# Optimization experiments

Measured on AMD Instinct MI355X. Metric: run time of the kernel, lower is better.

Reference implementation:

```python
import jax, jax.numpy as jnp
import numpy as np

NUM_HEADS = 8
WIN = 8

def setup_inputs() -> dict:
    key = jax.random.key(0)
    k1, k2, k3 = jax.random.split(key, 3)
    B, H, W, C = 4, 256, 256, 256
    x = jax.random.normal(k1, (B, H, W, C), dtype=jnp.float32)
    w_qkv = jax.random.normal(k2, (C, 3 * C), dtype=jnp.float32) * (1.0 / np.sqrt(C))
    b_qkv = jnp.zeros((3 * C,), dtype=jnp.float32)
    w_proj = jax.random.normal(k3, (C, C), dtype=jnp.float32) * (1.0 / np.sqrt(C))
    b_proj = jnp.zeros((C,), dtype=jnp.float32)
    return {"x": x, "w_qkv": w_qkv, "b_qkv": b_qkv, "w_proj": w_proj, "b_proj": b_proj}

def reference(x, w_qkv, b_qkv, w_proj, b_proj):
    B, H, W, C = x.shape
    ws = WIN
    pad_h = (ws - H % ws) % ws
    pad_w = (ws - W % ws) % ws
    if pad_h > 0 or pad_w > 0:
        x = jnp.pad(x, ((0, 0), (0, pad_h), (0, pad_w), (0, 0)), mode='reflect')
        H, W = H + pad_h, W + pad_w
    Ho, Wo = H - pad_h, W - pad_w
    # window partition: [B, H//ws, ws, W//ws, ws, C] -> [nW, ws*ws, C]
    xw = x.reshape(B, H // ws, ws, W // ws, ws, C)
    xw = xw.transpose(0, 1, 3, 2, 4, 5).reshape(-1, ws * ws, C)
    head_dim = C // NUM_HEADS
    scale = head_dim ** (-0.5)
    qkv = xw @ w_qkv + b_qkv  # [nW, T, 3C]
    qkv = qkv.reshape(-1, ws * ws, 3, NUM_HEADS, head_dim).transpose(2, 0, 3, 1, 4)
    q, k, v = qkv[0], qkv[1], qkv[2]  # each [nW, h, T, d]
    attn = jnp.einsum('whtd,whsd->whts', q, k) * scale
    attn = jax.nn.softmax(attn, axis=-1)
    o = jnp.einsum('whts,whsd->whtd', attn, v)
    o = o.transpose(0, 2, 1, 3).reshape(-1, ws * ws, C)
    o = o @ w_proj + b_proj
    # window merge
    o = o.reshape(B, H // ws, W // ws, ws, ws, C)
    o = o.transpose(0, 1, 3, 2, 4, 5).reshape(B, H, W, C)
    return o[:, :Ho, :Wo, :]
```

## Files before the change

### kernel.cpp

```cpp
#include <hip/hip_runtime.h>
#include <hip/hip_bf16.h>

typedef __attribute__((ext_vector_type(8))) short short8;
typedef __attribute__((ext_vector_type(4))) short short4v;
typedef __attribute__((ext_vector_type(4))) float f32x4;

#define MFMA(a, b, c) __builtin_amdgcn_mfma_f32_16x16x32_bf16(a, b, c, 0, 0, 0)
#define XS(t, c) (((t) << 8) + ((c) ^ (((t) & 7) << 3)))

extern "C" __device__ float __ocml_native_exp2_f32(float);
#define EXP2(x) __ocml_native_exp2_f32(x)

__device__ __forceinline__ unsigned int pk2(float lo, float hi) {
    union { __hip_bfloat162 h2; unsigned int u; } cv;
    cv.h2 = __float22bfloat162_rn(make_float2(lo, hi));
    return cv.u;
}

__device__ __forceinline__ unsigned short f2bf1(float f) {
    unsigned int u = __float_as_uint(f);
    u += 0x7FFFu + ((u >> 16) & 1u);
    return (unsigned short)(u >> 16);
}

__device__ __forceinline__ short4v u2s4(uint2 p) {
    union { uint2 u; short4v s; } t; t.u = p; return t.s;
}

#if __has_builtin(__builtin_amdgcn_mfma_f32_16x16x16bf16_1k)
__device__ __forceinline__ f32x4 mfma16(uint2 a, uint2 b, f32x4 c) {
    return __builtin_amdgcn_mfma_f32_16x16x16bf16_1k(u2s4(a), u2s4(b), c, 0, 0, 0);
}
#else
__device__ __forceinline__ short8 zfrag(uint2 p) {
    union { unsigned int u[4]; short8 s; } t;
    t.u[0] = p.x; t.u[1] = p.y; t.u[2] = 0u; t.u[3] = 0u;
    return t.s;
}
__device__ __forceinline__ f32x4 mfma16(uint2 a, uint2 b, f32x4 c) {
    return MFMA(zfrag(a), zfrag(b), c);
}
#endif

#define SCLF 0.25500566631879443f

__global__ void prep_w(const float* __restrict__ wqkv, const float* __restrict__ wproj,
                       unsigned short* __restrict__ wT) {
    int idx = blockIdx.x * 256 + threadIdx.x;
    if (idx < 196608) {
        const int frag   = idx >> 9;
        const int within = idx & 511;
        const int lane = within >> 3, j = within & 7;
        const int ks = frag & 7;
        const int dt = (frag >> 3) & 1;
        const int hh = (frag >> 4) & 7;
        const int m  = frag >> 7;
        const int n = m * 256 + hh * 32 + dt * 16 + (lane & 15);
        const int k = ks * 32 + ((lane >> 4) << 3) + j;
        float v = wqkv[k * 768 + n];
        if (m == 0) v *= SCLF;
        wT[idx] = f2bf1(v);
    } else {
        const int r = idx - 196608;
        const int frag = r >> 9;
        const int within = r & 511;
        const int lane = within >> 3, j = within & 7;
        const int ks = frag & 7;
        const int nt = (frag >> 3) & 1;
        const int hh = frag >> 4;
        const int n = hh * 32 + nt * 16 + (lane & 15);
        const int k = ks * 32 + ((lane >> 4) << 3) + j;
        wT[idx] = f2bf1(wproj[k * 256 + n]);
    }
}

__global__ __launch_bounds__(512, 2)
void winattn(const float* __restrict__ x,
             const float* __restrict__ bqkv,
             const float* __restrict__ bproj,
             const unsigned short* __restrict__ wpk,
             const unsigned short* __restrict__ wpj,
             float* __restrict__ out)
{
    __shared__ unsigned short smem[64 * 256];

    const int tid  = threadIdx.x;
    const int h    = tid >> 6;
    const int lane = tid & 63;
    const int g    = lane >> 4;
    const int q16  = lane & 15;

    const int bid  = blockIdx.x;
    const int widx = (bid & 7) * 512 + (bid >> 3);
    const int b  = widx >> 10;
    const int wh = (widx >> 5) & 31;
    const int ww = widx & 31;

    {
        const int t  = tid >> 3;
        const int c0 = (tid & 7) << 3;
        const int hr = (wh << 3) + (t >> 3);
        const int wc = (ww << 3) + (t & 7);
        const float* rowp = x + (((size_t)b * 256 + hr) * 256 + wc) * 256;
        #pragma unroll
        for (int u = 0; u < 4; ++u) {
            const int c = c0 + (u << 6);
            const float4 f0 = *reinterpret_cast<const float4*>(rowp + c);
            const float4 f1 = *reinterpret_cast<const float4*>(rowp + c + 4);
            union { unsigned int u4[4]; short8 s; } pv;
            pv.u4[0] = pk2(f0.x, f0.y); pv.u4[1] = pk2(f0.z, f0.w);
            pv.u4[2] = pk2(f1.x, f1.y); pv.u4[3] = pk2(f1.z, f1.w);
            *reinterpret_cast<short8*>(&smem[XS(t, c)]) = pv.s;
        }
    }
    __syncthreads();

    const unsigned short* wh0 = wpk + ((size_t)h << 13);
    const int loff = lane << 3;

    uint2 pq[2][4], pkk[2][4], pv2[2][4];
    #pragma unroll
    for (int half = 0; half < 2; ++half) {
        f32x4 acc[3][2][2];
        #pragma unroll
        for (int dt = 0; dt < 2; ++dt) {
            const float4 bbq = *reinterpret_cast<const float4*>(bqkv + h * 32 + dt * 16 + (g << 2));
            const float4 bbk = *reinterpret_cast<const float4*>(bqkv + 256 + h * 32 + dt * 16 + (g << 2));
            const float bv = bqkv[512 + h * 32 + dt * 16 + q16];
            const f32x4 iq = {bbq.x * SCLF, bbq.y * SCLF, bbq.z * SCLF, bbq.w * SCLF};
            const f32x4 ik = {bbk.x, bbk.y, bbk.z, bbk.w};
            const f32x4 ivv = {bv, bv, bv, bv};
            #pragma unroll
            for (int t2 = 0; t2 < 2; ++t2) {
                acc[0][dt][t2] = iq; acc[1][dt][t2] = ik; acc[2][dt][t2] = ivv;
            }
        }
        #pragma unroll
        for (int ks = 0; ks < 8; ++ks) {
            const int kc = ks << 5;
            short8 xf[2];
            #pragma unroll
            for (int t2 = 0; t2 < 2; ++t2)
                xf[t2] = *reinterpret_cast<const short8*>(
                    &smem[XS(((half << 1) + t2) * 16 + q16, kc + (g << 3))]);
            #pragma unroll
            for (int m = 0; m < 3; ++m) {
                #pragma unroll
                for (int dt = 0; dt < 2; ++dt) {
                    const short8 wf = *reinterpret_cast<const short8*>(
                        wh0 + (((size_t)m << 16) | (((dt << 3) + ks) << 9)) + loff);
                    #pragma unroll
                    for (int t2 = 0; t2 < 2; ++t2)
                        acc[m][dt][t2] = (m < 2) ? MFMA(wf, xf[t2], acc[m][dt][t2])
                                                 : MFMA(xf[t2], wf, acc[m][dt][t2]);
                }
            }
        }
        #pragma unroll
        for (int dt = 0; dt < 2; ++dt) {
            #pragma unroll
            for (int t2 = 0; t2 < 2; ++t2) {
                const int tt = (half << 1) + t2;
                const f32x4 aq = acc[0][dt][t2];
                pq[dt][tt]  = make_uint2(pk2(aq[0], aq[1]), pk2(aq[2], aq[3]));
                const f32x4 ak = acc[1][dt][t2];
                pkk[dt][tt] = make_uint2(pk2(ak[0], ak[1]), pk2(ak[2], ak[3]));
                const f32x4 av = acc[2][dt][t2];
                pv2[dt][tt] = make_uint2(pk2(av[0], av[1]), pk2(av[2], av[3]));
            }
        }
    }

    const f32x4 fz = {0.f, 0.f, 0.f, 0.f};
    uint2 ppk[4][4];
    float inv4[4];
    #pragma unroll
    for (int qt = 0; qt < 4; ++qt) {
        f32x4 st[4];
        #pragma unroll
        for (int kt = 0; kt < 4; ++kt) st[kt] = fz;
        #pragma unroll
        for (int dt = 0; dt < 2; ++dt)
            #pragma unroll
            for (int kt = 0; kt < 4; ++kt)
                st[kt] = mfma16(pkk[dt][kt], pq[dt][qt], st[kt]);
        float sum = 0.f;
        #pragma unroll
        for (int kt = 0; kt < 4; ++kt) {
            const float e0 = EXP2(st[kt][0]), e1 = EXP2(st[kt][1]);
            const float e2 = EXP2(st[kt][2]), e3 = EXP2(st[kt][3]);
            sum += (e0 + e1) + (e2 + e3);
            ppk[kt][qt] = make_uint2(pk2(e0, e1), pk2(e2, e3));
        }
        sum += __shfl_xor(sum, 16);
        sum += __shfl_xor(sum, 32);
        inv4[qt] = 1.f / sum;
    }

    f32x4 ot[2][4];
    #pragma unroll
    for (int dt = 0; dt < 2; ++dt)
        #pragma unroll
        for (int tt = 0; tt < 4; ++tt) ot[dt][tt] = fz;
    #pragma unroll
    for (int kt = 0; kt < 4; ++kt)
        #pragma unroll
        for (int tt = 0; tt < 4; ++tt)
            #pragma unroll
            for (int dt = 0; dt < 2; ++dt)
                ot[dt][tt] = mfma16(pv2[dt][kt], ppk[kt][tt], ot[dt][tt]);

    __syncthreads();
    #pragma unroll
    for (int dt = 0; dt < 2; ++dt)
        #pragma unroll
        for (int tt = 0; tt < 4; ++tt) {
            const float iv = inv4[tt];
            const int tok = tt * 16 + q16;
            const int d   = h * 32 + dt * 16 + (g << 2);
            const uint2 pv = make_uint2(pk2(ot[dt][tt][0] * iv, ot[dt][tt][1] * iv),
                                        pk2(ot[dt][tt][2] * iv, ot[dt][tt][3] * iv));
            *reinterpret_cast<uint2*>(&smem[XS(tok, d)]) = pv;
        }
    __syncthreads();

    f32x4 pacc[4][2];
    {
        float bpv[2];
        #pragma unroll
        for (int nt = 0; nt < 2; ++nt) bpv[nt] = bproj[h * 32 + nt * 16 + q16];
        #pragma unroll
        for (int mt = 0; mt < 4; ++mt)
            #pragma unroll
            for (int nt = 0; nt < 2; ++nt) {
                const f32x4 ib = {bpv[nt], bpv[nt], bpv[nt], bpv[nt]};
                pacc[mt][nt] = ib;
            }
    }
    const unsigned short* wpjh = wpj + ((size_t)h << 13);
    #pragma unroll
    for (int ks = 0; ks < 8; ++ks) {
        const int kc = ks << 5;
        short8 of[4], wf[2];
        #pragma unroll
        for (int mt = 0; mt < 4; ++mt)
            of[mt] = *reinterpret_cast<const short8*>(&smem[XS(mt * 16 + q16, kc + (g << 3))]);
        #pragma unroll
        for (int nt = 0; nt < 2; ++nt)
            wf[nt] = *reinterpret_cast<const short8*>(wpjh + (((nt << 3) + ks) << 9) + loff);
        #pragma unroll
        for (int mt = 0; mt < 4; ++mt)
            #pragma unroll
            for (int nt = 0; nt < 2; ++nt)
                pacc[mt][nt] = MFMA(of[mt], wf[nt], pacc[mt][nt]);
    }
    {
        float* obase = out + (((size_t)b * 256 + (wh << 3) + (g >> 1)) * 256
                              + (ww << 3) + ((g & 1) << 2)) * 256 + h * 32 + q16;
        #pragma unroll
        for (int mt = 0; mt < 4; ++mt)
            #pragma unroll
            for (int r = 0; r < 4; ++r)
                #pragma unroll
                for (int nt = 0; nt < 2; ++nt)
                    obase[mt * 131072 + r * 256 + nt * 16] = pacc[mt][nt][r];
    }
}

extern "C" void kernel_launch(void* const* d_in, const int* in_sizes, int n_in,
                              void* d_out, int out_size, void* d_ws, size_t ws_size,
                              hipStream_t stream) {
    const float* x     = (const float*)d_in[0];
    const float* wqkv  = (const float*)d_in[1];
    const float* bqkv  = (const float*)d_in[2];
    const float* wproj = (const float*)d_in[3];
    const float* bproj = (const float*)d_in[4];
    float* out = (float*)d_out;
    unsigned short* wT = (unsigned short*)d_ws;

    prep_w<<<1024, 256, 0, stream>>>(wqkv, wproj, wT);
    winattn<<<4096, 512, 0, stream>>>(x, bqkv, bproj, wT, wT + 196608, out);
}
```

Measured before the change: 291.1 us.

## Use 4-wave blocks with each wave processing two heads sequentially

The block drops from 8 waves to 4. Each wave now loops over two heads for the QKV projection and attention, and writes its per-head outputs into a separate LDS region. That removes one barrier between attention and the projection stage. The output projection is re-partitioned so each wave computes 64 output columns, and the wproj prepack layout is changed to match. LDS per block doubles to 64KB and per-wave work doubles, which may cut occupancy and latency hiding in exchange for fewer waves and less sync.

```diff
diff --git a/kernel.cpp b/kernel.cpp
--- a/kernel.cpp
+++ b/kernel.cpp
@@ -66,15 +66,14 @@
         const int within = r & 511;
         const int lane = within >> 3, j = within & 7;
         const int ks = frag & 7;
-        const int nt = (frag >> 3) & 1;
-        const int hh = frag >> 4;
-        const int n = hh * 32 + nt * 16 + (lane & 15);
+        const int cb = frag >> 3;
+        const int n = cb * 16 + (lane & 15);
         const int k = ks * 32 + ((lane >> 4) << 3) + j;
         wT[idx] = f2bf1(wproj[k * 256 + n]);
     }
 }
 
-__global__ __launch_bounds__(512, 2)
+__global__ __launch_bounds__(256, 2)
 void winattn(const float* __restrict__ x,
              const float* __restrict__ bqkv,
              const float* __restrict__ bproj,
@@ -82,10 +81,10 @@
              const unsigned short* __restrict__ wpj,
              float* __restrict__ out)
 {
-    __shared__ unsigned short smem[64 * 256];
+    __shared__ unsigned short smem[32768];
 
     const int tid  = threadIdx.x;
-    const int h    = tid >> 6;
+    const int wid  = tid >> 6;
     const int lane = tid & 63;
     const int g    = lane >> 4;
     const int q16  = lane & 15;
@@ -97,14 +96,14 @@
     const int ww = widx & 31;
 
     {
-        const int t  = tid >> 3;
-        const int c0 = (tid & 7) << 3;
+        const int t  = tid >> 2;
+        const int c0 = (tid & 3) << 3;
         const int hr = (wh << 3) + (t >> 3);
         const int wc = (ww << 3) + (t & 7);
         const float* rowp = x + (((size_t)b * 256 + hr) * 256 + wc) * 256;
         #pragma unroll
-        for (int u = 0; u < 4; ++u) {
-            const int c = c0 + (u << 6);
+        for (int u = 0; u < 8; ++u) {
+            const int c = c0 + (u << 5);
             const float4 f0 = *reinterpret_cast<const float4*>(rowp + c);
             const float4 f1 = *reinterpret_cast<const float4*>(rowp + c + 4);
             union { unsigned int u4[4]; short8 s; } pv;
@@ -115,154 +114,158 @@
     }
     __syncthreads();
 
-    const unsigned short* wh0 = wpk + ((size_t)h << 13);
+    const f32x4 fz = {0.f, 0.f, 0.f, 0.f};
     const int loff = lane << 3;
 
-    uint2 pq[2][4], pkk[2][4], pv2[2][4];
-    #pragma unroll
-    for (int half = 0; half < 2; ++half) {
-        f32x4 acc[3][2][2];
-        #pragma unroll
-        for (int dt = 0; dt < 2; ++dt) {
-            const float4 bbq = *reinterpret_cast<const float4*>(bqkv + h * 32 + dt * 16 + (g << 2));
-            const float4 bbk = *reinterpret_cast<const float4*>(bqkv + 256 + h * 32 + dt * 16 + (g << 2));
-            const float bv = bqkv[512 + h * 32 + dt * 16 + q16];
-            const f32x4 iq = {bbq.x * SCLF, bbq.y * SCLF, bbq.z * SCLF, bbq.w * SCLF};
-            const f32x4 ik = {bbk.x, bbk.y, bbk.z, bbk.w};
-            const f32x4 ivv = {bv, bv, bv, bv};
-            #pragma unroll
-            for (int t2 = 0; t2 < 2; ++t2) {
-                acc[0][dt][t2] = iq; acc[1][dt][t2] = ik; acc[2][dt][t2] = ivv;
-            }
-        }
-        #pragma unroll
-        for (int ks = 0; ks < 8; ++ks) {
-            const int kc = ks << 5;
-            short8 xf[2];
-            #pragma unroll
-            for (int t2 = 0; t2 < 2; ++t2)
-                xf[t2] = *reinterpret_cast<const short8*>(
-                    &smem[XS(((half << 1) + t2) * 16 + q16, kc + (g << 3))]);
-            #pragma unroll
-            for (int m = 0; m < 3; ++m) {
-                #pragma unroll
-                for (int dt = 0; dt < 2; ++dt) {
-                    const short8 wf = *reinterpret_cast<const short8*>(
-                        wh0 + (((size_t)m << 16) | (((dt << 3) + ks) << 9)) + loff);
+    #pragma unroll 1
+    for (int p = 0; p < 2; ++p) {
+        const int h = (p << 2) + wid;
+        const unsigned short* wh0 = wpk + ((size_t)h << 13);
+
+        uint2 pq[2][4], pkk[2][4], pv2[2][4];
+        #pragma unroll
+        for (int half = 0; half < 2; ++half) {
+            f32x4 acc[3][2][2];
+            #pragma unroll
+            for (int dt = 0; dt < 2; ++dt) {
+                const float4 bbq = *reinterpret_cast<const float4*>(bqkv + h * 32 + dt * 16 + (g << 2));
+                const float4 bbk = *reinterpret_cast<const float4*>(bqkv + 256 + h * 32 + dt * 16 + (g << 2));
+                const float bv = bqkv[512 + h * 32 + dt * 16 + q16];
+                const f32x4 iq = {bbq.x * SCLF, bbq.y * SCLF, bbq.z * SCLF, bbq.w * SCLF};
+                const f32x4 ik = {bbk.x, bbk.y, bbk.z, bbk.w};
+                const f32x4 ivv = {bv, bv, bv, bv};
+                #pragma unroll
+                for (int t2 = 0; t2 < 2; ++t2) {
+                    acc[0][dt][t2] = iq; acc[1][dt][t2] = ik; acc[2][dt][t2] = ivv;
+                }
+            }
+            #pragma unroll
+            for (int ks = 0; ks < 8; ++ks) {
+                const int kc = ks << 5;
+                short8 xf[2];
+                #pragma unroll
+                for (int t2 = 0; t2 < 2; ++t2)
+                    xf[t2] = *reinterpret_cast<const short8*>(
+                        &smem[XS(((half << 1) + t2) * 16 + q16, kc + (g << 3))]);
+                #pragma unroll
+                for (int m = 0; m < 3; ++m) {
                     #pragma unroll
-                    for (int t2 = 0; t2 < 2; ++t2)
-                        acc[m][dt][t2] = (m < 2) ? MFMA(wf, xf[t2], acc[m][dt][t2])
-                                                 : MFMA(xf[t2], wf, acc[m][dt][t2]);
+                    for (int dt = 0; dt < 2; ++dt) {
+                        const short8 wf = *reinterpret_cast<const short8*>(
+                            wh0 + (((size_t)m << 16) | (((dt << 3) + ks) << 9)) + loff);
+                        #pragma unroll
+                        for (int t2 = 0; t2 < 2; ++t2)
+                            acc[m][dt][t2] = (m < 2) ? MFMA(wf, xf[t2], acc[m][dt][t2])
+                                                     : MFMA(xf[t2], wf, acc[m][dt][t2]);
+                    }
                 }
             }
-        }
-        #pragma unroll
-        for (int dt = 0; dt < 2; ++dt) {
-            #pragma unroll
-            for (int t2 = 0; t2 < 2; ++t2) {
-                const int tt = (half << 1) + t2;
-                const f32x4 aq = acc[0][dt][t2];
-                pq[dt][tt]  = make_uint2(pk2(aq[0], aq[1]), pk2(aq[2], aq[3]));
-                const f32x4 ak = acc[1][dt][t2];
-                pkk[dt][tt] = make_uint2(pk2(ak[0], ak[1]), pk2(ak[2], ak[3]));
-                const f32x4 av = acc[2][dt][t2];
-                pv2[dt][tt] = make_uint2(pk2(av[0], av[1]), pk2(av[2], av[3]));
-            }
-        }
-    }
-
-    const f32x4 fz = {0.f, 0.f, 0.f, 0.f};
-    uint2 ppk[4][4];
-    float inv4[4];
-    #pragma unroll
-    for (int qt = 0; qt < 4; ++qt) {
-        f32x4 st[4];
-        #pragma unroll
-        for (int kt = 0; kt < 4; ++kt) st[kt] = fz;
+            #pragma unroll
+            for (int dt = 0; dt < 2; ++dt) {
+                #pragma unroll
+                for (int t2 = 0; t2 < 2; ++t2) {
+                    const int tt = (half << 1) + t2;
+                    const f32x4 aq = acc[0][dt][t2];
+                    pq[dt][tt]  = make_uint2(pk2(aq[0], aq[1]), pk2(aq[2], aq[3]));
+                    const f32x4 ak = acc[1][dt][t2];
+                    pkk[dt][tt] = make_uint2(pk2(ak[0], ak[1]), pk2(ak[2], ak[3]));
+                    const f32x4 av = acc[2][dt][t2];
+                    pv2[dt][tt] = make_uint2(pk2(av[0], av[1]), pk2(av[2], av[3]));
+                }
+            }
+        }
+
+        uint2 ppk[4][4];
+        float inv4[4];
+        #pragma unroll
+        for (int qt = 0; qt < 4; ++qt) {
+            f32x4 st[4];
+            #pragma unroll
+            for (int kt = 0; kt < 4; ++kt) st[kt] = fz;
+            #pragma unroll
+            for (int dt = 0; dt < 2; ++dt)
+                #pragma unroll
+                for (int kt = 0; kt < 4; ++kt)
+                    st[kt] = mfma16(pkk[dt][kt], pq[dt][qt], st[kt]);
+            float sum = 0.f;
+            #pragma unroll
+            for (int kt = 0; kt < 4; ++kt) {
+                const float e0 = EXP2(st[kt][0]), e1 = EXP2(st[kt][1]);
+                const float e2 = EXP2(st[kt][2]), e3 = EXP2(st[kt][3]);
+                sum += (e0 + e1) + (e2 + e3);
+                ppk[kt][qt] = make_uint2(pk2(e0, e1), pk2(e2, e3));
+            }
+            sum += __shfl_xor(sum, 16);
+            sum += __shfl_xor(sum, 32);
+            inv4[qt] = 1.f / sum;
+        }
+
+        f32x4 ot[2][4];
         #pragma unroll
         for (int dt = 0; dt < 2; ++dt)
             #pragma unroll
-            for (int kt = 0; kt < 4; ++kt)
-                st[kt] = mfma16(pkk[dt][kt], pq[dt][qt], st[kt]);
-        float sum = 0.f;
-        #pragma unroll
-        for (int kt = 0; kt < 4; ++kt) {
-            const float e0 = EXP2(st[kt][0]), e1 = EXP2(st[kt][1]);
-            const float e2 = EXP2(st[kt][2]), e3 = EXP2(st[kt][3]);
-            sum += (e0 + e1) + (e2 + e3);
-            ppk[kt][qt] = make_uint2(pk2(e0, e1), pk2(e2, e3));
-        }
-        sum += __shfl_xor(sum, 16);
-        sum += __shfl_xor(sum, 32);
-        inv4[qt] = 1.f / sum;
-    }
-
-    f32x4 ot[2][4];
-    #pragma unroll
-    for (int dt = 0; dt < 2; ++dt)
-        #pragma unroll
-        for (int tt = 0; tt < 4; ++tt) ot[dt][tt] = fz;
-    #pragma unroll
-    for (int kt = 0; kt < 4; ++kt)
-        #pragma unroll
-        for (int tt = 0; tt < 4; ++tt)
-            #pragma unroll
-            for (int dt = 0; dt < 2; ++dt)
-                ot[dt][tt] = mfma16(pv2[dt][kt], ppk[kt][tt], ot[dt][tt]);
-
+            for (int tt = 0; tt < 4; ++tt) ot[dt][tt] = fz;
+        #pragma unroll
+        for (int kt = 0; kt < 4; ++kt)
+            #pragma unroll
+            for (int tt = 0; tt < 4; ++tt)
+                #pragma unroll
+                for (int dt = 0; dt < 2; ++dt)
+                    ot[dt][tt] = mfma16(pv2[dt][kt], ppk[kt][tt], ot[dt][tt]);
+
+        #pragma unroll
+        for (int dt = 0; dt < 2; ++dt)
+            #pragma unroll
+            for (int tt = 0; tt < 4; ++tt) {
+                const float iv = inv4[tt];
+                const int tok = tt * 16 + q16;
+                const int d   = h * 32 + dt * 16 + (g << 2);
+                const uint2 pv = make_uint2(pk2(ot[dt][tt][0] * iv, ot[dt][tt][1] * iv),
+                                            pk2(ot[dt][tt][2] * iv, ot[dt][tt][3] * iv));
+                *reinterpret_cast<uint2*>(&smem[16384 + XS(tok, d)]) = pv;
+            }
+    }
     __syncthreads();
-    #pragma unroll
-    for (int dt = 0; dt < 2; ++dt)
-        #pragma unroll
-        for (int tt = 0; tt < 4; ++tt) {
-            const float iv = inv4[tt];
-            const int tok = tt * 16 + q16;
-            const int d   = h * 32 + dt * 16 + (g << 2);
-            const uint2 pv = make_uint2(pk2(ot[dt][tt][0] * iv, ot[dt][tt][1] * iv),
-                                        pk2(ot[dt][tt][2] * iv, ot[dt][tt][3] * iv));
-            *reinterpret_cast<uint2*>(&smem[XS(tok, d)]) = pv;
-        }
-    __syncthreads();
-
-    f32x4 pacc[4][2];
+
+    f32x4 pacc[4][4];
     {
-        float bpv[2];
-        #pragma unroll
-        for (int nt = 0; nt < 2; ++nt) bpv[nt] = bproj[h * 32 + nt * 16 + q16];
-        #pragma unroll
-        for (int mt = 0; mt < 4; ++mt)
-            #pragma unroll
-            for (int nt = 0; nt < 2; ++nt) {
-                const f32x4 ib = {bpv[nt], bpv[nt], bpv[nt], bpv[nt]};
-                pacc[mt][nt] = ib;
-            }
-    }
-    const unsigned short* wpjh = wpj + ((size_t)h << 13);
+        #pragma unroll
+        for (int nt = 0; nt < 4; ++nt) {
+            const float bpv = bproj[wid * 64 + nt * 16 + q16];
+            const f32x4 ib = {bpv, bpv, bpv, bpv};
+            #pragma unroll
+            for (int mt = 0; mt < 4; ++mt) pacc[mt][nt] = ib;
+        }
+    }
     #pragma unroll
     for (int ks = 0; ks < 8; ++ks) {
         const int kc = ks << 5;
-        short8 of[4], wf[2];
+        short8 of[4], wf[4];
         #pragma unroll
         for (int mt = 0; mt < 4; ++mt)
-            of[mt] = *reinterpret_cast<const short8*>(&smem[XS(mt * 16 + q16, kc + (g << 3))]);
-        #pragma unroll
-        for (int nt = 0; nt < 2; ++nt)
-            wf[nt] = *reinterpret_cast<const short8*>(wpjh + (((nt << 3) + ks) << 9) + loff);
+            of[mt] = *reinterpret_cast<const short8*>(
+                &smem[16384 + XS(mt * 16 + q16, kc + (g << 3))]);
+        #pragma unroll
+        for (int nt = 0; nt < 4; ++nt) {
+            const int cb = (wid << 2) + nt;
+            wf[nt] = *reinterpret_cast<const short8*>(
+                wpj + (cb << 12) + (ks << 9) + loff);
+        }
         #pragma unroll
         for (int mt = 0; mt < 4; ++mt)
             #pragma unroll
-            for (int nt = 0; nt < 2; ++nt)
+            for (int nt = 0; nt < 4; ++nt)
                 pacc[mt][nt] = MFMA(of[mt], wf[nt], pacc[mt][nt]);
     }
     {
         float* obase = out + (((size_t)b * 256 + (wh << 3) + (g >> 1)) * 256
-                              + (ww << 3) + ((g & 1) << 2)) * 256 + h * 32 + q16;
+                              + (ww << 3) + ((g & 1) << 2)) * 256 + wid * 64 + q16;
         #pragma unroll
         for (int mt = 0; mt < 4; ++mt)
             #pragma unroll
             for (int r = 0; r < 4; ++r)
                 #pragma unroll
-                for (int nt = 0; nt < 2; ++nt)
+                for (int nt = 0; nt < 4; ++nt)
                     obase[mt * 131072 + r * 256 + nt * 16] = pacc[mt][nt][r];
     }
 }
@@ -279,5 +282,5 @@
     unsigned short* wT = (unsigned short*)d_ws;
 
     prep_w<<<1024, 256, 0, stream>>>(wqkv, wproj, wT);
-    winattn<<<4096, 512, 0, stream>>>(x, bqkv, bproj, wT, wT + 196608, out);
-}
+    winattn<<<4096, 256, 0, stream>>>(x, bqkv, bproj, wT, wT + 196608, out);
+}
```

Measured after the change: 390.1 us. 1.34x slower.
